# Optimization experiments

Measured on AMD Instinct MI355X. Metric: run time of the kernel, lower is better.

The kernel has to match this reference:

```python
import jax, jax.numpy as jnp
import numpy as np

N = 25000   # num nodes
E = 500000  # num edges
B = 4       # num queries (batch)
D = 32      # hidden dim
R2 = 474    # doubled num_relation
L = 4       # num conv layers
EPS = 1e-6


def setup_inputs() -> dict:
    key = jax.random.key(0)
    ks = jax.random.split(key, 12)
    return {
        "node_in": jax.random.randint(ks[0], (E,), 0, N),
        "node_out": jax.random.randint(ks[1], (E,), 0, N),
        "relation": jax.random.randint(ks[2], (E,), 0, R2),
        "edge_weight": jnp.ones((E,), jnp.float32),
        "h_index": jax.random.randint(ks[3], (B,), 0, N),
        "r_index": jax.random.randint(ks[4], (B,), 0, R2),
        "query_embed": jax.random.normal(ks[5], (R2, D), jnp.float32) * 0.1,
        "rel_W": jax.random.normal(ks[6], (L, D, R2 * D), jnp.float32) * 0.05,
        "rel_b": jnp.zeros((L, R2 * D), jnp.float32),
        "lin_W": jax.random.normal(ks[7], (L, 13 * D, D), jnp.float32) * 0.05,
        "lin_b": jnp.zeros((L, D), jnp.float32),
        "mlp_W1": jax.random.normal(ks[8], (2 * D, 2 * D), jnp.float32) * 0.05,
        "mlp_b1": jnp.zeros((2 * D,), jnp.float32),
        "mlp_W2": jax.random.normal(ks[9], (2 * D, 1), jnp.float32) * 0.05,
        "mlp_b2": jnp.zeros((1,), jnp.float32),
    }


def _nbfnet(node_in, node_out, relation, h_index, r_index,
            edge_weight, query_embed, rel_W, rel_b, lin_W, lin_b,
            mlp_W1, mlp_b1, mlp_W2, mlp_b2):
    query = query_embed[r_index]                                   # [B, D]
    # boundary condition: query embedding placed at the head node of each query
    boundary = jnp.zeros((N, B, D), query.dtype).at[h_index, jnp.arange(B)].set(query)
    # append one self-entry per node (boundary message), as in the torch code
    node_out_ext = jnp.concatenate([node_out, jnp.arange(N)])      # [E+N]
    w_ext = jnp.concatenate([edge_weight, jnp.ones((N,), edge_weight.dtype)])[:, None, None]
    cnt = jax.ops.segment_sum(jnp.ones((E + N,), query.dtype), node_out_ext, N)[:, None, None]
    deg = jax.ops.segment_sum(edge_weight, node_out, N) + 1.0      # degree_out + 1, [N]
    scale = jnp.log(deg)
    scale = scale / scale.mean()
    scales = jnp.stack([jnp.ones_like(scale), scale, 1.0 / jnp.clip(scale, 0.01)], -1)  # [N,3]

    hidden = boundary
    for l in range(L):
        # dependent relation embeddings: [R2, B, D]
        rel_in = (query @ rel_W[l] + rel_b[l]).reshape(B, R2, D).transpose(1, 0, 2)
        # distmult message + boundary self-message: [E+N, B, D]
        msg = jnp.concatenate([rel_in[relation] * hidden[node_in], boundary], 0)
        mw = msg * w_ext
        mean = jax.ops.segment_sum(mw, node_out_ext, N) / cnt
        sq_mean = jax.ops.segment_sum(msg * mw, node_out_ext, N) / cnt
        mx = jax.ops.segment_max(mw, node_out_ext, N)
        mn = jax.ops.segment_min(mw, node_out_ext, N)
        std = jnp.sqrt(jnp.clip(sq_mean - mean * mean, EPS))
        feat = jnp.stack([mean, mx, mn, std], -1).reshape(N, B, 4 * D)   # PNA stats
        update = (feat[..., None] * scales[:, None, None, :]).reshape(N, B, 12 * D)
        hidden = jax.nn.relu(jnp.concatenate([hidden, update], -1) @ lin_W[l] + lin_b[l])

    feat = jnp.concatenate([hidden, jnp.broadcast_to(query[None], (N, B, D))], -1)  # [N,B,2D]
    h1 = jax.nn.relu(feat @ mlp_W1 + mlp_b1)
    score = (h1 @ mlp_W2 + mlp_b2)[..., 0]                          # [N, B]
    return score.T                                                  # [B, N]


def reference(node_in, node_out, relation, edge_weight, h_index, r_index,
              query_embed, rel_W, rel_b, lin_W, lin_b,
              mlp_W1, mlp_b1, mlp_W2, mlp_b2):
    return _nbfnet(node_in, node_out, relation, h_index, r_index,
                   edge_weight, query_embed, rel_W, rel_b, lin_W, lin_b,
                   mlp_W1, mlp_b1, mlp_W2, mlp_b2)
```

## Files before the change

### kernel.cpp

```cpp
#include <hip/hip_runtime.h>
#include <hip/hip_fp16.h>

#define NN  25000
#define EE  500000
#define BB  4
#define DD  32
#define LL  4
#define R2C 474
#define BD  128
#define THD 416
#define EPSF 1e-6f
#define WMH 13312

typedef _Float16 half8 __attribute__((ext_vector_type(8)));
typedef float    f32x4 __attribute__((ext_vector_type(4)));

__global__ __launch_bounds__(256) void pidx_kernel(const int* __restrict__ node_out,
                                                   int* __restrict__ cnt,
                                                   int* __restrict__ pidx) {
  int e = blockIdx.x * 256 + threadIdx.x;
  if (e < EE) pidx[e] = atomicAdd(&cnt[node_out[e]], 1);
}

__global__ __launch_bounds__(256) void prep_kernel(const int* __restrict__ cnt,
                                                   int* __restrict__ base,
                                                   float* __restrict__ cntf,
                                                   int* __restrict__ gcnt) {
  int n = blockIdx.x * 256 + threadIdx.x;
  if (n >= NN) return;
  int c = cnt[n];
  base[n] = atomicAdd(gcnt, (c + 1) & ~1);
  cntf[n] = (float)(c + 1);
}

__global__ __launch_bounds__(256) void scatter_kernel(const int* __restrict__ node_in,
                                                      const int* __restrict__ node_out,
                                                      const int* __restrict__ relation,
                                                      const float* __restrict__ ew,
                                                      const int* __restrict__ base,
                                                      const int* __restrict__ pidx,
                                                      int2* __restrict__ ep) {
  int e = blockIdx.x * 256 + threadIdx.x;
  if (e >= EE) return;
  int pos = base[node_out[e]] + pidx[e];
  ep[pos] = make_int2(node_in[e] | (relation[e] << 15), __float_as_int(ew[e]));
}

__global__ __launch_bounds__(256) void wdeg_kernel(const int* __restrict__ base,
                                                   const int* __restrict__ cnt,
                                                   const int2* __restrict__ ep,
                                                   float* __restrict__ lg,
                                                   float* __restrict__ logsum) {
  int n = blockIdx.x * 256 + threadIdx.x;
  float v = 0.f;
  if (n < NN) {
    int b = base[n], c = cnt[n];
    float s = 0.f;
    for (int p = b; p < b + c; ++p) s += __int_as_float(ep[p].y);
    v = logf(s + 1.0f);
    lg[n] = v;
  }
  __shared__ float red[256];
  red[threadIdx.x] = v; __syncthreads();
  for (int o = 128; o > 0; o >>= 1) {
    if (threadIdx.x < o) red[threadIdx.x] += red[threadIdx.x + o];
    __syncthreads();
  }
  if (threadIdx.x == 0) atomicAdd(logsum, red[0]);
}

__global__ __launch_bounds__(256) void scales_kernel(const float* __restrict__ lg,
                                                     const float* __restrict__ logsum,
                                                     float* __restrict__ scales) {
  int n = blockIdx.x * 256 + threadIdx.x;
  if (n >= NN) return;
  float mean = logsum[0] / (float)NN;
  float sc = lg[n] / mean;
  scales[n * 2 + 0] = sc;
  scales[n * 2 + 1] = 1.0f / fmaxf(sc, 0.01f);
}

__global__ __launch_bounds__(128) void init_kernel(const int* __restrict__ h_index,
                                                   const int* __restrict__ r_index,
                                                   const float* __restrict__ qemb,
                                                   float* __restrict__ query,
                                                   __half* __restrict__ h0) {
  int t = threadIdx.x; int b = t >> 5, d = t & 31;
  float qv = qemb[r_index[b] * DD + d];
  query[t] = qv;
  h0[h_index[b] * BD + t] = __float2half(qv);
}

__global__ __launch_bounds__(256) void relin_all_kernel(const float* __restrict__ query,
                                                        const float* __restrict__ relW,
                                                        const float* __restrict__ relB,
                                                        __half* __restrict__ relIn) {
  int o = blockIdx.x * 256 + threadIdx.x;
  if (o >= LL * R2C * BD) return;
  int l = o / (R2C * BD);
  int rest = o % (R2C * BD);
  int r = rest >> 7, b = (rest >> 5) & 3, d = rest & 31;
  int col = r * DD + d;
  const float* W = relW + (size_t)l * DD * R2C * DD;
  float acc = relB[(size_t)l * R2C * DD + col];
  #pragma unroll
  for (int k = 0; k < DD; ++k)
    acc = fmaf(query[b * DD + k], W[(size_t)k * (R2C * DD) + col], acc);
  relIn[o] = __float2half(acc);
}

__global__ __launch_bounds__(256) void wmbuild_kernel(const float* __restrict__ linW,
                                                      _Float16* __restrict__ Wm) {
  int idx = blockIdx.x * 256 + threadIdx.x;
  if (idx >= LL * WMH) return;
  int l = idx / WMH, rest = idx % WMH;
  int t = rest >> 10;
  int nt = (rest >> 9) & 1;
  int L = (rest >> 3) & 63;
  int j = rest & 7;
  int k = t * 32 + (L >> 4) * 8 + j;
  int n = nt * 16 + (L & 15);
  int wrow;
  if (k < 32) wrow = k;
  else {
    int kk = k - 32;
    int slab = kk >> 7, s = (kk >> 5) & 3, dd = kk & 31;
    wrow = DD + (dd * 4 + s) * 3 + slab;
  }
  Wm[idx] = (_Float16)linW[(size_t)l * THD * DD + (size_t)wrow * DD + n];
}

__global__ __launch_bounds__(256) void gather_kernel(const __half2* __restrict__ hin2,
                                                     const __half2* __restrict__ rel2,
                                                     const int2* __restrict__ ep,
                                                     const int* __restrict__ base,
                                                     const int* __restrict__ cnt,
                                                     const float* __restrict__ cntf,
                                                     const int* __restrict__ h_index,
                                                     const float* __restrict__ query,
                                                     __half2* __restrict__ statsH) {
  const int lane = threadIdx.x & 63;
  const int n = blockIdx.x * 4 + (threadIdx.x >> 6);
  const int b = lane >> 4;
  const int d0 = (lane & 15) * 2;
  const float q0 = query[b * 32 + d0], q1 = query[b * 32 + d0 + 1];
  const int hb = h_index[b];
  const int beg = __builtin_amdgcn_readfirstlane(base[n]);
  const int cnn = __builtin_amdgcn_readfirstlane(cnt[n]);
  const float mb0 = (n == hb) ? q0 : 0.f;
  const float mb1 = (n == hb) ? q1 : 0.f;
  float sa0 = mb0, qa0 = mb0 * mb0, mx0 = mb0, mn0 = mb0;
  float sa1 = mb1, qa1 = mb1 * mb1, mx1 = mb1, mn1 = mb1;

#define PROC(Ez, Hv, Rv) {                                                   \
    float w = __int_as_float(Ez);                                            \
    float2 hf = __half22float2(Hv), rf = __half22float2(Rv);                 \
    float m0 = rf.x * hf.x, mw0 = m0 * w;                                    \
    float m1 = rf.y * hf.y, mw1 = m1 * w;                                    \
    sa0 += mw0; qa0 = fmaf(m0, mw0, qa0);                                    \
    mx0 = fmaxf(mx0, mw0); mn0 = fminf(mn0, mw0);                            \
    sa1 += mw1; qa1 = fmaf(m1, mw1, qa1);                                    \
    mx1 = fmaxf(mx1, mw1); mn1 = fminf(mn1, mw1); }
#define ROWS(Ex, Hd, Rd) {                                                   \
    Hd = hin2[(unsigned)((Ex) & 0x7fff) * 64 + lane];                        \
    Rd = rel2[(unsigned)((unsigned)(Ex) >> 15) * 64 + lane]; }

  int p = beg;
  int rem = cnn;
  const int nb = rem >> 3;
  if (nb > 0) {
    int2 E0, E1, E2, E3, E4, E5, E6, E7;
    __half2 H0, H1, H2, H3, H4, H5, H6, H7;
    __half2 R0, R1, R2, R3, R4, R5, R6, R7;
    E0 = ep[p];     E1 = ep[p + 1]; E2 = ep[p + 2]; E3 = ep[p + 3];
    E4 = ep[p + 4]; E5 = ep[p + 5]; E6 = ep[p + 6]; E7 = ep[p + 7];
    ROWS(E0.x, H0, R0); ROWS(E1.x, H1, R1); ROWS(E2.x, H2, R2); ROWS(E3.x, H3, R3);
    ROWS(E4.x, H4, R4); ROWS(E5.x, H5, R5); ROWS(E6.x, H6, R6); ROWS(E7.x, H7, R7);
    for (int it = 1; it < nb; ++it) {
      const int pn = p + 8;
      int2 F0 = ep[pn],     F1 = ep[pn + 1], F2 = ep[pn + 2], F3 = ep[pn + 3];
      int2 F4 = ep[pn + 4], F5 = ep[pn + 5], F6 = ep[pn + 6], F7 = ep[pn + 7];
      __half2 G0, G1, G2, G3, G4, G5, G6, G7;
      __half2 S0, S1, S2, S3, S4, S5, S6, S7;
      ROWS(F0.x, G0, S0); ROWS(F1.x, G1, S1); ROWS(F2.x, G2, S2); ROWS(F3.x, G3, S3);
      ROWS(F4.x, G4, S4); ROWS(F5.x, G5, S5); ROWS(F6.x, G6, S6); ROWS(F7.x, G7, S7);
      PROC(E0.y, H0, R0); PROC(E1.y, H1, R1); PROC(E2.y, H2, R2); PROC(E3.y, H3, R3);
      PROC(E4.y, H4, R4); PROC(E5.y, H5, R5); PROC(E6.y, H6, R6); PROC(E7.y, H7, R7);
      E0 = F0; E1 = F1; E2 = F2; E3 = F3; E4 = F4; E5 = F5; E6 = F6; E7 = F7;
      H0 = G0; H1 = G1; H2 = G2; H3 = G3; H4 = G4; H5 = G5; H6 = G6; H7 = G7;
      R0 = S0; R1 = S1; R2 = S2; R3 = S3; R4 = S4; R5 = S5; R6 = S6; R7 = S7;
      p = pn;
    }
    PROC(E0.y, H0, R0); PROC(E1.y, H1, R1); PROC(E2.y, H2, R2); PROC(E3.y, H3, R3);
    PROC(E4.y, H4, R4); PROC(E5.y, H5, R5); PROC(E6.y, H6, R6); PROC(E7.y, H7, R7);
    p += 8;
    rem -= nb << 3;
  }
  if (rem >= 4) {
    int2 E0 = ep[p], E1 = ep[p + 1], E2 = ep[p + 2], E3 = ep[p + 3];
    __half2 H0, H1, H2, H3, R0, R1, R2, R3;
    ROWS(E0.x, H0, R0); ROWS(E1.x, H1, R1); ROWS(E2.x, H2, R2); ROWS(E3.x, H3, R3);
    PROC(E0.y, H0, R0); PROC(E1.y, H1, R1); PROC(E2.y, H2, R2); PROC(E3.y, H3, R3);
    p += 4; rem -= 4;
  }
  for (; rem > 0; --rem, ++p) {
    int2 e = ep[p];
    __half2 hv, rv;
    ROWS(e.x, hv, rv);
    PROC(e.y, hv, rv);
  }
#undef ROWS
#undef PROC
  const float invc = 1.0f / cntf[n];
  const float mean0 = sa0 * invc, mean1 = sa1 * invc;
  const float sd0 = sqrtf(fmaxf(qa0 * invc - mean0 * mean0, EPSF));
  const float sd1 = sqrtf(fmaxf(qa1 * invc - mean1 * mean1, EPSF));
  __half2* sp = statsH + (unsigned)n * 256 + lane;
  sp[0]   = __floats2half2_rn(mean0, mean1);
  sp[64]  = __floats2half2_rn(mx0, mx1);
  sp[128] = __floats2half2_rn(mn0, mn1);
  sp[192] = __floats2half2_rn(sd0, sd1);
}

__global__ __launch_bounds__(128) void mfma_linear_kernel(const _Float16* __restrict__ hinh,
                                                          __half* __restrict__ houth,
                                                          const _Float16* __restrict__ statsH,
                                                          const float* __restrict__ scales,
                                                          const _Float16* __restrict__ Wm,
                                                          const float* __restrict__ bias) {
  const int lane = threadIdx.x & 63;
  const int wid  = threadIdx.x >> 6;
  const int nbase = blockIdx.x * 8 + wid * 4;
  const int m = lane & 15;
  const int q = lane >> 4;
  const int n = nbase + (m >> 2);
  const int b = m & 3;
  const _Float16 one = (_Float16)1.f;
  const _Float16 s1h = (_Float16)scales[n * 2 + 0];
  const _Float16 s2h = (_Float16)scales[n * 2 + 1];
  const _Float16* hsrc = hinh   + (unsigned)n * BD  + b * 32 + q * 8;
  const _Float16* ssrc = statsH + (unsigned)n * 512 + b * 32 + q * 8;

  f32x4 c0 = {0.f, 0.f, 0.f, 0.f};
  f32x4 c1 = {0.f, 0.f, 0.f, 0.f};
  #pragma unroll
  for (int t = 0; t < 13; ++t) {
    half8 a;
    if (t == 0) {
      a = *(const half8*)hsrc;
    } else {
      const int slab = (t - 1) >> 2, s = (t - 1) & 3;
      a = *(const half8*)(ssrc + s * 128);
      const _Float16 sc = (slab == 0) ? one : ((slab == 1) ? s1h : s2h);
      half8 sv = {sc, sc, sc, sc, sc, sc, sc, sc};
      a = a * sv;
    }
    half8 b0 = *(const half8*)(Wm + (unsigned)(t * 2 + 0) * 512 + lane * 8);
    half8 b1 = *(const half8*)(Wm + (unsigned)(t * 2 + 1) * 512 + lane * 8);
    c0 = __builtin_amdgcn_mfma_f32_16x16x32_f16(a, b0, c0, 0, 0, 0);
    c1 = __builtin_amdgcn_mfma_f32_16x16x32_f16(a, b1, c1, 0, 0, 0);
  }
  const int col = lane & 15;
  const float bj0 = bias[col], bj1 = bias[col + 16];
  #pragma unroll
  for (int i = 0; i < 4; ++i) {
    const int mr = q * 4 + i;
    const int nl = mr >> 2, bq = mr & 3;
    __half* dst = houth + (unsigned)(nbase + nl) * BD + bq * 32 + col;
    dst[0]  = __float2half(fmaxf(c0[i] + bj0, 0.f));
    dst[16] = __float2half(fmaxf(c1[i] + bj1, 0.f));
  }
}

__global__ __launch_bounds__(128) void mlp_kernel(const __half* __restrict__ hinh,
                                                  const float* __restrict__ query,
                                                  const float* __restrict__ W1,
                                                  const float* __restrict__ b1,
                                                  const float* __restrict__ W2,
                                                  const float* __restrict__ b2,
                                                  float* __restrict__ out) {
  __shared__ float f2[BB][2 * DD];
  const int t = threadIdx.x;
  const int b = t >> 5, d = t & 31;
  const float qv = query[t];
  const float w2a = W2[d], w2b = W2[DD + d];
  const float b1a = b1[d], b1b = b1[DD + d];
  const float b2v = b2[0];
  const int NPBM = 8;
  int n0 = blockIdx.x * NPBM, n1 = min(n0 + NPBM, NN);
  for (int n = n0; n < n1; ++n) {
    f2[b][d]      = __half2float(hinh[(unsigned)n * BD + t]);
    f2[b][DD + d] = qv;
    float a0 = b1a, a1 = b1b;
    #pragma unroll
    for (int i = 0; i < 2 * DD; ++i) {
      float v = f2[b][i];
      a0 = fmaf(v, W1[i * 2 * DD + d], a0);
      a1 = fmaf(v, W1[i * 2 * DD + DD + d], a1);
    }
    a0 = fmaxf(a0, 0.f); a1 = fmaxf(a1, 0.f);
    float part = a0 * w2a + a1 * w2b;
    #pragma unroll
    for (int off = 16; off > 0; off >>= 1) part += __shfl_down(part, off, 32);
    if (d == 0) out[b * NN + n] = part + b2v;
  }
}

extern "C" void kernel_launch(void* const* d_in, const int* in_sizes, int n_in,
                              void* d_out, int out_size, void* d_ws, size_t ws_size,
                              hipStream_t stream) {
  const int*   node_in  = (const int*)d_in[0];
  const int*   node_out = (const int*)d_in[1];
  const int*   relation = (const int*)d_in[2];
  const float* ew       = (const float*)d_in[3];
  const int*   h_index  = (const int*)d_in[4];
  const int*   r_index  = (const int*)d_in[5];
  const float* qemb     = (const float*)d_in[6];
  const float* relW     = (const float*)d_in[7];
  const float* relB     = (const float*)d_in[8];
  const float* linW     = (const float*)d_in[9];
  const float* linB     = (const float*)d_in[10];
  const float* W1       = (const float*)d_in[11];
  const float* b1       = (const float*)d_in[12];
  const float* W2       = (const float*)d_in[13];
  const float* b2       = (const float*)d_in[14];
  float* out = (float*)d_out;

  char* ws = (char*)d_ws;
  size_t off = 0;
  auto alloc = [&](size_t bytes) -> char* {
    char* p = ws + off;
    off += (bytes + 255) & ~(size_t)255;
    return p;
  };
  __half*   h0     = (__half*)  alloc((size_t)NN * BD * 2);
  __half*   h1     = (__half*)  alloc((size_t)NN * BD * 2);
  __half*   relIn  = (__half*)  alloc((size_t)LL * R2C * BD * 2);
  __half*   statsH = (__half*)  alloc((size_t)NN * 512 * 2);
  _Float16* Wm     = (_Float16*)alloc((size_t)LL * WMH * 2);
  int2*     ep     = (int2*)    alloc(((size_t)EE + NN) * 8);
  int*      pidx   = (int*)     alloc((size_t)EE * 4);
  int*      base   = (int*)     alloc((size_t)NN * 4);
  int*      cnti   = (int*)     alloc((size_t)NN * 4);
  float*    lg     = (float*)   alloc((size_t)NN * 4);
  float*    cntf   = (float*)   alloc((size_t)NN * 4);
  float*    scales = (float*)   alloc((size_t)NN * 2 * 4);
  float*    query  = (float*)   alloc((size_t)BD * 4);
  float*    stats  = (float*)   alloc(256);

  hipMemsetAsync(cnti, 0, (size_t)NN * 4, stream);
  hipMemsetAsync(stats, 0, 256, stream);
  hipMemsetAsync(h0,   0, (size_t)NN * BD * 2, stream);

  float* logsum = stats;
  int*   gcnt   = (int*)stats + 1;

  pidx_kernel   <<<(EE + 255) / 256, 256, 0, stream>>>(node_out, cnti, pidx);
  prep_kernel   <<<(NN + 255) / 256, 256, 0, stream>>>(cnti, base, cntf, gcnt);
  scatter_kernel<<<(EE + 255) / 256, 256, 0, stream>>>(node_in, node_out, relation, ew,
                                                       base, pidx, ep);
  wdeg_kernel   <<<(NN + 255) / 256, 256, 0, stream>>>(base, cnti, ep, lg, logsum);
  scales_kernel <<<(NN + 255) / 256, 256, 0, stream>>>(lg, logsum, scales);
  init_kernel   <<<1, 128, 0, stream>>>(h_index, r_index, qemb, query, h0);
  wmbuild_kernel<<<(LL * WMH + 255) / 256, 256, 0, stream>>>(linW, Wm);
  relin_all_kernel<<<(LL * R2C * BD + 255) / 256, 256, 0, stream>>>(query, relW, relB, relIn);

  __half* hin = h0; __half* hout = h1;
  for (int l = 0; l < LL; ++l) {
    gather_kernel<<<NN / 4, 256, 0, stream>>>(
        (const __half2*)hin, (const __half2*)relIn + (size_t)l * R2C * 64,
        ep, base, cnti, cntf, h_index, query, (__half2*)statsH);
    mfma_linear_kernel<<<NN / 8, 128, 0, stream>>>(
        (const _Float16*)hin, hout, (const _Float16*)statsH, scales,
        Wm + (size_t)l * WMH, linB + (size_t)l * DD);
    __half* tmp = hin; hin = hout; hout = tmp;
  }
  mlp_kernel<<<(NN + 7) / 8, 128, 0, stream>>>(hin, query, W1, b1, W2, b2, out);
}
```

Before: 313.4 us.

## Specialize first-layer gather for sparse boundary, vectorize CSR build, fold scales

Adds a layer-0 gather kernel that exploits the fact that the initial hidden state is non-zero only at each query's head node. It therefore skips loading hidden rows and only fetches relation rows for edges whose source equals the head node. It also vectorizes the pidx and scatter CSR-build kernels to process four edges per thread with int4 loads. It removes the separate scales kernel by computing degree scales inline in the linear kernel. The layer-0 specialization relies on the boundary structure, which holds for any input, but it bakes one branchy path per query lane and assumes node ids fit in 15 bits.

After: 302.5 us. -3.5%, faster.

```diff
diff --git a/kernel.cpp b/kernel.cpp
--- a/kernel.cpp
+++ b/kernel.cpp
@@ -15,11 +15,18 @@
 typedef _Float16 half8 __attribute__((ext_vector_type(8)));
 typedef float    f32x4 __attribute__((ext_vector_type(4)));
 
-__global__ __launch_bounds__(256) void pidx_kernel(const int* __restrict__ node_out,
+__global__ __launch_bounds__(256) void pidx_kernel(const int4* __restrict__ no4,
                                                    int* __restrict__ cnt,
-                                                   int* __restrict__ pidx) {
-  int e = blockIdx.x * 256 + threadIdx.x;
-  if (e < EE) pidx[e] = atomicAdd(&cnt[node_out[e]], 1);
+                                                   int4* __restrict__ pidx4) {
+  int i = blockIdx.x * 256 + threadIdx.x;
+  if (i >= EE / 4) return;
+  int4 d = no4[i];
+  int4 r;
+  r.x = atomicAdd(&cnt[d.x], 1);
+  r.y = atomicAdd(&cnt[d.y], 1);
+  r.z = atomicAdd(&cnt[d.z], 1);
+  r.w = atomicAdd(&cnt[d.w], 1);
+  pidx4[i] = r;
 }
 
 __global__ __launch_bounds__(256) void prep_kernel(const int* __restrict__ cnt,
@@ -33,17 +40,21 @@
   cntf[n] = (float)(c + 1);
 }
 
-__global__ __launch_bounds__(256) void scatter_kernel(const int* __restrict__ node_in,
-                                                      const int* __restrict__ node_out,
-                                                      const int* __restrict__ relation,
-                                                      const float* __restrict__ ew,
+__global__ __launch_bounds__(256) void scatter_kernel(const int4* __restrict__ ni4,
+                                                      const int4* __restrict__ no4,
+                                                      const int4* __restrict__ rl4,
+                                                      const float4* __restrict__ ew4,
                                                       const int* __restrict__ base,
-                                                      const int* __restrict__ pidx,
+                                                      const int4* __restrict__ pidx4,
                                                       int2* __restrict__ ep) {
-  int e = blockIdx.x * 256 + threadIdx.x;
-  if (e >= EE) return;
-  int pos = base[node_out[e]] + pidx[e];
-  ep[pos] = make_int2(node_in[e] | (relation[e] << 15), __float_as_int(ew[e]));
+  int i = blockIdx.x * 256 + threadIdx.x;
+  if (i >= EE / 4) return;
+  int4 ni = ni4[i], no = no4[i], rl = rl4[i], pi = pidx4[i];
+  float4 w = ew4[i];
+  ep[base[no.x] + pi.x] = make_int2(ni.x | (rl.x << 15), __float_as_int(w.x));
+  ep[base[no.y] + pi.y] = make_int2(ni.y | (rl.y << 15), __float_as_int(w.y));
+  ep[base[no.z] + pi.z] = make_int2(ni.z | (rl.z << 15), __float_as_int(w.z));
+  ep[base[no.w] + pi.w] = make_int2(ni.w | (rl.w << 15), __float_as_int(w.w));
 }
 
 __global__ __launch_bounds__(256) void wdeg_kernel(const int* __restrict__ base,
@@ -67,17 +78,6 @@
     __syncthreads();
   }
   if (threadIdx.x == 0) atomicAdd(logsum, red[0]);
-}
-
-__global__ __launch_bounds__(256) void scales_kernel(const float* __restrict__ lg,
-                                                     const float* __restrict__ logsum,
-                                                     float* __restrict__ scales) {
-  int n = blockIdx.x * 256 + threadIdx.x;
-  if (n >= NN) return;
-  float mean = logsum[0] / (float)NN;
-  float sc = lg[n] / mean;
-  scales[n * 2 + 0] = sc;
-  scales[n * 2 + 1] = 1.0f / fmaxf(sc, 0.01f);
 }
 
 __global__ __launch_bounds__(128) void init_kernel(const int* __restrict__ h_index,
@@ -128,6 +128,56 @@
     wrow = DD + (dd * 4 + s) * 3 + slab;
   }
   Wm[idx] = (_Float16)linW[(size_t)l * THD * DD + (size_t)wrow * DD + n];
+}
+
+__global__ __launch_bounds__(256) void gather1_kernel(const __half2* __restrict__ rel2,
+                                                      const int2* __restrict__ ep,
+                                                      const int* __restrict__ base,
+                                                      const int* __restrict__ cnt,
+                                                      const float* __restrict__ cntf,
+                                                      const int* __restrict__ h_index,
+                                                      const float* __restrict__ query,
+                                                      __half2* __restrict__ statsH) {
+  const int lane = threadIdx.x & 63;
+  const int n = blockIdx.x * 4 + (threadIdx.x >> 6);
+  const int b = lane >> 4;
+  const int d0 = (lane & 15) * 2;
+  const float q0 = query[b * 32 + d0], q1 = query[b * 32 + d0 + 1];
+  const int hb = h_index[b];
+  const int beg = __builtin_amdgcn_readfirstlane(base[n]);
+  const int cnn = __builtin_amdgcn_readfirstlane(cnt[n]);
+  const float mb0 = (n == hb) ? q0 : 0.f;
+  const float mb1 = (n == hb) ? q1 : 0.f;
+  float sa0 = mb0, qa0 = mb0 * mb0, mx0 = mb0, mn0 = mb0;
+  float sa1 = mb1, qa1 = mb1 * mb1, mx1 = mb1, mn1 = mb1;
+  int matched = 0;
+  for (int p = beg; p < beg + cnn; ++p) {
+    int2 e = ep[p];
+    int src = e.x & 0x7fff;
+    if (src == hb) {
+      __half2 rv = rel2[(unsigned)((unsigned)e.x >> 15) * 64 + lane];
+      float w = __int_as_float(e.y);
+      float2 rf = __half22float2(rv);
+      float m0 = rf.x * q0, mw0 = m0 * w;
+      float m1 = rf.y * q1, mw1 = m1 * w;
+      sa0 += mw0; qa0 = fmaf(m0, mw0, qa0); mx0 = fmaxf(mx0, mw0); mn0 = fminf(mn0, mw0);
+      sa1 += mw1; qa1 = fmaf(m1, mw1, qa1); mx1 = fmaxf(mx1, mw1); mn1 = fminf(mn1, mw1);
+      ++matched;
+    }
+  }
+  if (matched < cnn) {
+    mx0 = fmaxf(mx0, 0.f); mn0 = fminf(mn0, 0.f);
+    mx1 = fmaxf(mx1, 0.f); mn1 = fminf(mn1, 0.f);
+  }
+  const float invc = 1.0f / cntf[n];
+  const float mean0 = sa0 * invc, mean1 = sa1 * invc;
+  const float sd0 = sqrtf(fmaxf(qa0 * invc - mean0 * mean0, EPSF));
+  const float sd1 = sqrtf(fmaxf(qa1 * invc - mean1 * mean1, EPSF));
+  __half2* sp = statsH + (unsigned)n * 256 + lane;
+  sp[0]   = __floats2half2_rn(mean0, mean1);
+  sp[64]  = __floats2half2_rn(mx0, mx1);
+  sp[128] = __floats2half2_rn(mn0, mn1);
+  sp[192] = __floats2half2_rn(sd0, sd1);
 }
 
 __global__ __launch_bounds__(256) void gather_kernel(const __half2* __restrict__ hin2,
@@ -225,7 +275,8 @@
 __global__ __launch_bounds__(128) void mfma_linear_kernel(const _Float16* __restrict__ hinh,
                                                           __half* __restrict__ houth,
                                                           const _Float16* __restrict__ statsH,
-                                                          const float* __restrict__ scales,
+                                                          const float* __restrict__ lg,
+                                                          const float* __restrict__ logsum,
                                                           const _Float16* __restrict__ Wm,
                                                           const float* __restrict__ bias) {
   const int lane = threadIdx.x & 63;
@@ -235,9 +286,11 @@
   const int q = lane >> 4;
   const int n = nbase + (m >> 2);
   const int b = m & 3;
+  const float invmean = (float)NN / logsum[0];
+  const float sc = lg[n] * invmean;
   const _Float16 one = (_Float16)1.f;
-  const _Float16 s1h = (_Float16)scales[n * 2 + 0];
-  const _Float16 s2h = (_Float16)scales[n * 2 + 1];
+  const _Float16 s1h = (_Float16)sc;
+  const _Float16 s2h = (_Float16)(1.0f / fmaxf(sc, 0.01f));
   const _Float16* hsrc = hinh   + (unsigned)n * BD  + b * 32 + q * 8;
   const _Float16* ssrc = statsH + (unsigned)n * 512 + b * 32 + q * 8;
 
@@ -251,8 +304,8 @@
     } else {
       const int slab = (t - 1) >> 2, s = (t - 1) & 3;
       a = *(const half8*)(ssrc + s * 128);
-      const _Float16 sc = (slab == 0) ? one : ((slab == 1) ? s1h : s2h);
-      half8 sv = {sc, sc, sc, sc, sc, sc, sc, sc};
+      const _Float16 sch = (slab == 0) ? one : ((slab == 1) ? s1h : s2h);
+      half8 sv = {sch, sch, sch, sch, sch, sch, sch, sch};
       a = a * sv;
     }
     half8 b0 = *(const half8*)(Wm + (unsigned)(t * 2 + 0) * 512 + lane * 8);
@@ -344,7 +397,6 @@
   int*      cnti   = (int*)     alloc((size_t)NN * 4);
   float*    lg     = (float*)   alloc((size_t)NN * 4);
   float*    cntf   = (float*)   alloc((size_t)NN * 4);
-  float*    scales = (float*)   alloc((size_t)NN * 2 * 4);
   float*    query  = (float*)   alloc((size_t)BD * 4);
   float*    stats  = (float*)   alloc(256);
 
@@ -355,23 +407,30 @@
   float* logsum = stats;
   int*   gcnt   = (int*)stats + 1;
 
-  pidx_kernel   <<<(EE + 255) / 256, 256, 0, stream>>>(node_out, cnti, pidx);
+  pidx_kernel   <<<(EE / 4 + 255) / 256, 256, 0, stream>>>((const int4*)node_out,
+                                                           cnti, (int4*)pidx);
   prep_kernel   <<<(NN + 255) / 256, 256, 0, stream>>>(cnti, base, cntf, gcnt);
-  scatter_kernel<<<(EE + 255) / 256, 256, 0, stream>>>(node_in, node_out, relation, ew,
-                                                       base, pidx, ep);
+  scatter_kernel<<<(EE / 4 + 255) / 256, 256, 0, stream>>>(
+      (const int4*)node_in, (const int4*)node_out, (const int4*)relation,
+      (const float4*)ew, base, (const int4*)pidx, ep);
   wdeg_kernel   <<<(NN + 255) / 256, 256, 0, stream>>>(base, cnti, ep, lg, logsum);
-  scales_kernel <<<(NN + 255) / 256, 256, 0, stream>>>(lg, logsum, scales);
   init_kernel   <<<1, 128, 0, stream>>>(h_index, r_index, qemb, query, h0);
   wmbuild_kernel<<<(LL * WMH + 255) / 256, 256, 0, stream>>>(linW, Wm);
   relin_all_kernel<<<(LL * R2C * BD + 255) / 256, 256, 0, stream>>>(query, relW, relB, relIn);
 
   __half* hin = h0; __half* hout = h1;
   for (int l = 0; l < LL; ++l) {
-    gather_kernel<<<NN / 4, 256, 0, stream>>>(
-        (const __half2*)hin, (const __half2*)relIn + (size_t)l * R2C * 64,
-        ep, base, cnti, cntf, h_index, query, (__half2*)statsH);
+    if (l == 0) {
+      gather1_kernel<<<NN / 4, 256, 0, stream>>>(
+          (const __half2*)relIn, ep, base, cnti, cntf, h_index, query,
+          (__half2*)statsH);
+    } else {
+      gather_kernel<<<NN / 4, 256, 0, stream>>>(
+          (const __half2*)hin, (const __half2*)relIn + (size_t)l * R2C * 64,
+          ep, base, cnti, cntf, h_index, query, (__half2*)statsH);
+    }
     mfma_linear_kernel<<<NN / 8, 128, 0, stream>>>(
-        (const _Float16*)hin, hout, (const _Float16*)statsH, scales,
+        (const _Float16*)hin, hout, (const _Float16*)statsH, lg, logsum,
         Wm + (size_t)l * WMH, linB + (size_t)l * DD);
     __half* tmp = hin; hin = hout; hout = tmp;
   }
```
